# Kernel tuning notes

Measured on AMD Instinct MI355X. Metric: run time of the kernel, lower is better.

## Reference

```python
import jax, jax.numpy as jnp
import numpy as np

H = 64           # num_attention_heads
DH = 96          # attention_head_size = 6144/64
DM = 6144        # hidden_size


def setup_inputs() -> dict:
    key = jax.random.key(0)
    ks = jax.random.split(key, 7)
    s = 1.0 / np.sqrt(DM)
    return {
        "hidden_states": jax.random.normal(ks[0], (1, 2048, DM), dtype=jnp.float32),
        "Wq": jax.random.uniform(ks[1], (DM, DM), jnp.float32, -s, s),
        "bq": jax.random.uniform(ks[2], (DM,), jnp.float32, -s, s),
        "Wk": jax.random.uniform(ks[3], (DM, DM), jnp.float32, -s, s),
        "bk": jax.random.uniform(ks[4], (DM,), jnp.float32, -s, s),
        "Wv": jax.random.uniform(ks[5], (DM, DM), jnp.float32, -s, s),
        "bv": jax.random.uniform(ks[6], (DM,), jnp.float32, -s, s),
    }


def reference(hidden_states, Wq, bq, Wk, bk, Wv, bv):
    B, S, _ = hidden_states.shape

    def split_heads(x):  # [B,S,DM] -> [B,H,S,DH]
        return x.reshape(B, S, H, DH).transpose(0, 2, 1, 3)

    q = split_heads(hidden_states @ Wq + bq)
    k = split_heads(hidden_states @ Wk + bk)
    v = split_heads(hidden_states @ Wv + bv)

    scores = jnp.einsum("bhqd,bhkd->bhqk", q, k) / np.sqrt(DH).astype(np.float32)
    probs = jax.nn.softmax(scores, axis=-1)  # dropout p=0.0005 -> eval identity
    ctx = jnp.einsum("bhqk,bhkd->bhqd", probs, v)
    ctx = ctx.transpose(0, 2, 1, 3).reshape(B, S, H * DH)
    return ctx
```

## Files before the change

kernel.cpp:

```cpp
#include <hip/hip_runtime.h>
#include <hip/hip_bf16.h>
#include <stdint.h>


#define NH  64
#define DHD 96
#define DM  6144
#define SEQ 2048

typedef __attribute__((ext_vector_type(4))) float f4;
typedef __attribute__((ext_vector_type(4))) float f32x4;
typedef __attribute__((ext_vector_type(8))) short bf16x8;
typedef __attribute__((ext_vector_type(4))) short bf16x4;

static __device__ __forceinline__ short f2bf(float f) {
  unsigned int u = __builtin_bit_cast(unsigned int, f);
  u = (u + 0x7fffu + ((u >> 16) & 1u)) >> 16;
  return (short)u;
}

__global__ __launch_bounds__(256)
void qkv_gemm(const float* __restrict__ hs,
              const float* __restrict__ Wq, const float* __restrict__ bq,
              const float* __restrict__ Wk, const float* __restrict__ bk,
              const float* __restrict__ Wv, const float* __restrict__ bv,
              short* __restrict__ Qo, short* __restrict__ Ko, short* __restrict__ Vto)
{
  const int z = blockIdx.z;
  const float* __restrict__ Wp = (z == 0) ? Wq : ((z == 1) ? Wk : Wv);
  const float* __restrict__ bp = (z == 0) ? bq : ((z == 1) ? bk : bv);

  const int tid  = threadIdx.x;
  const int lane = tid & 63;
  const int w    = tid >> 6;
  const int wr   = w >> 1, wc = w & 1;
  const int g    = lane >> 4, c = lane & 15;
  const int m0   = blockIdx.y * 128;
  const int n0   = blockIdx.x * 128;

  __shared__ short Al[128 * 72];
  __shared__ short Bl[128 * 72];

  f32x4 acc[4][4];
#pragma unroll
  for (int i = 0; i < 4; ++i)
#pragma unroll
    for (int j = 0; j < 4; ++j) acc[i][j] = (f32x4)0.f;

  const int nb  = tid & 31;
  const int kb8 = tid >> 5;

  f4 areg[8];
  f4 breg[8];

  {
#pragma unroll
    for (int i = 0; i < 4; ++i) {
      int o = tid * 32 + i * 8192;
      int row = o >> 8, colf = (o & 255) >> 2;
      const float* p = hs + (size_t)(m0 + row) * DM + colf;
      areg[2*i]   = *(const f4*)p;
      areg[2*i+1] = *(const f4*)(p + 4);
    }
#pragma unroll
    for (int kk = 0; kk < 8; ++kk)
      breg[kk] = *(const f4*)(Wp + (size_t)(kb8*8 + kk) * DM + n0 + nb*4);
  }

  for (int kt = 0; kt < DM/64; ++kt) {
#pragma unroll
    for (int i = 0; i < 4; ++i) {
      int o = tid * 32 + i * 8192;
      int row = o >> 8, colf = (o & 255) >> 2;
      bf16x8 v;
      v[0]=f2bf(areg[2*i][0]);   v[1]=f2bf(areg[2*i][1]);
      v[2]=f2bf(areg[2*i][2]);   v[3]=f2bf(areg[2*i][3]);
      v[4]=f2bf(areg[2*i+1][0]); v[5]=f2bf(areg[2*i+1][1]);
      v[6]=f2bf(areg[2*i+1][2]); v[7]=f2bf(areg[2*i+1][3]);
      *(bf16x8*)&Al[row * 72 + colf] = v;
    }
#pragma unroll
    for (int nn = 0; nn < 4; ++nn) {
      bf16x8 v;
#pragma unroll
      for (int kk = 0; kk < 8; ++kk) v[kk] = f2bf(breg[kk][nn]);
      *(bf16x8*)&Bl[(nb*4 + nn) * 72 + kb8*8] = v;
    }
    __syncthreads();

    if (kt + 1 < DM/64) {
      const int k0 = (kt + 1) * 64;
#pragma unroll
      for (int i = 0; i < 4; ++i) {
        int o = tid * 32 + i * 8192;
        int row = o >> 8, colf = (o & 255) >> 2;
        const float* p = hs + (size_t)(m0 + row) * DM + k0 + colf;
        areg[2*i]   = *(const f4*)p;
        areg[2*i+1] = *(const f4*)(p + 4);
      }
#pragma unroll
      for (int kk = 0; kk < 8; ++kk)
        breg[kk] = *(const f4*)(Wp + (size_t)(k0 + kb8*8 + kk) * DM + n0 + nb*4);
    }

#pragma unroll
    for (int kh = 0; kh < 2; ++kh) {
      bf16x8 af[4], bfr[4];
#pragma unroll
      for (int i = 0; i < 4; ++i)
        af[i]  = *(bf16x8*)&Al[(wr*64 + i*16 + c) * 72 + kh*32 + g*8];
#pragma unroll
      for (int j = 0; j < 4; ++j)
        bfr[j] = *(bf16x8*)&Bl[(wc*64 + j*16 + c) * 72 + kh*32 + g*8];
#pragma unroll
      for (int i = 0; i < 4; ++i)
#pragma unroll
        for (int j = 0; j < 4; ++j)
          acc[i][j] = __builtin_amdgcn_mfma_f32_16x16x32_bf16(af[i], bfr[j], acc[i][j], 0, 0, 0);
    }
    __syncthreads();
  }

  if (z < 2) {
    short* __restrict__ outp = (z == 0) ? Qo : Ko;
#pragma unroll
    for (int j = 0; j < 4; ++j) {
      int n = n0 + wc*64 + j*16 + c;
      int hh = n / DHD, d = n - hh * DHD;
      float bias = bp[n];
      short* ob = outp + (size_t)hh * SEQ * DHD + d;
#pragma unroll
      for (int i = 0; i < 4; ++i) {
        int srow = m0 + wr*64 + i*16 + g*4;
#pragma unroll
        for (int r = 0; r < 4; ++r)
          ob[(size_t)(srow + r) * DHD] = f2bf(acc[i][j][r] + bias);
      }
    }
  } else {
#pragma unroll
    for (int j = 0; j < 4; ++j) {
      int n = n0 + wc*64 + j*16 + c;
      int hh = n / DHD, d = n - hh * DHD;
      float bias = bp[n];
      short* ob = Vto + ((size_t)hh * DHD + d) * SEQ;
#pragma unroll
      for (int i = 0; i < 4; ++i) {
        int srow = m0 + wr*64 + i*16 + g*4;
        bf16x4 v;
        v[0]=f2bf(acc[i][j][0]+bias); v[1]=f2bf(acc[i][j][1]+bias);
        v[2]=f2bf(acc[i][j][2]+bias); v[3]=f2bf(acc[i][j][3]+bias);
        *(bf16x4*)&ob[srow] = v;
      }
    }
  }
}

__global__ __launch_bounds__(256)
void attn_fwd(const short* __restrict__ Qo, const short* __restrict__ Ko,
              const short* __restrict__ Vto, float* __restrict__ out)
{
  const int h  = blockIdx.y;
  const int q0 = blockIdx.x * 64;
  const int tid = threadIdx.x, lane = tid & 63, w = tid >> 6;
  const int g = lane >> 4, c = lane & 15;

  __shared__ short Ql[64 * 104];
  __shared__ short Kl[64 * 104];
  __shared__ short Vl[96 * 72];
  __shared__ short Pl[64 * 72];

  const short* __restrict__ Qh = Qo  + (size_t)h * SEQ * DHD;
  const short* __restrict__ Kh = Ko  + (size_t)h * SEQ * DHD;
  const short* __restrict__ Vh = Vto + (size_t)h * DHD * SEQ;

#pragma unroll
  for (int j = 0; j < 3; ++j) {
    int i = tid + j * 256;
    int row = i / 12, cb = (i % 12) * 8;
    *(int4*)&Ql[row * 104 + cb] = *(const int4*)(Qh + (size_t)(q0 + row) * DHD + cb);
  }
  __syncthreads();

  bf16x8 qf[3];
#pragma unroll
  for (int dc = 0; dc < 3; ++dc)
    qf[dc] = *(bf16x8*)&Ql[(w*16 + c) * 104 + dc*32 + g*8];

  f32x4 octx[6];
#pragma unroll
  for (int i = 0; i < 6; ++i) octx[i] = (f32x4)0.f;
  float mrun = -__builtin_inff();
  float lrun = 0.f;
  const float rs = 0.10206207261596577f;

  for (int kv = 0; kv < SEQ/64; ++kv) {
    const int s0 = kv * 64;
    int4 kreg[3], vreg[3];
#pragma unroll
    for (int j = 0; j < 3; ++j) {
      int i = tid + j * 256;
      int krow = i / 12, kcb = (i % 12) * 8;
      kreg[j] = *(const int4*)(Kh + (size_t)(s0 + krow) * DHD + kcb);
      int vrow = i >> 3, vcb = (i & 7) * 8;
      vreg[j] = *(const int4*)(Vh + (size_t)vrow * SEQ + s0 + vcb);
    }
    __syncthreads();
#pragma unroll
    for (int j = 0; j < 3; ++j) {
      int i = tid + j * 256;
      int krow = i / 12, kcb = (i % 12) * 8;
      *(int4*)&Kl[krow * 104 + kcb] = kreg[j];
      int vrow = i >> 3, vcb = (i & 7) * 8;
      *(int4*)&Vl[vrow * 72 + vcb] = vreg[j];
    }
    __syncthreads();

    f32x4 sc[4];
#pragma unroll
    for (int kt = 0; kt < 4; ++kt) {
      sc[kt] = (f32x4)0.f;
#pragma unroll
      for (int dc = 0; dc < 3; ++dc) {
        bf16x8 kf = *(bf16x8*)&Kl[(kt*16 + c) * 104 + dc*32 + g*8];
        sc[kt] = __builtin_amdgcn_mfma_f32_16x16x32_bf16(kf, qf[dc], sc[kt], 0, 0, 0);
      }
    }

    float tmax = -__builtin_inff();
#pragma unroll
    for (int kt = 0; kt < 4; ++kt)
#pragma unroll
      for (int r = 0; r < 4; ++r) { sc[kt][r] *= rs; tmax = fmaxf(tmax, sc[kt][r]); }
    tmax = fmaxf(tmax, __shfl_xor(tmax, 16));
    tmax = fmaxf(tmax, __shfl_xor(tmax, 32));
    float mnew = fmaxf(mrun, tmax);
    float cs = __expf(mrun - mnew);
    float p[4][4];
    float psum = 0.f;
#pragma unroll
    for (int kt = 0; kt < 4; ++kt)
#pragma unroll
      for (int r = 0; r < 4; ++r) { p[kt][r] = __expf(sc[kt][r] - mnew); psum += p[kt][r]; }
    psum += __shfl_xor(psum, 16);
    psum += __shfl_xor(psum, 32);
    lrun = lrun * cs + psum;
    mrun = mnew;

    float csr[4];
#pragma unroll
    for (int r = 0; r < 4; ++r) csr[r] = __shfl(cs, g*4 + r, 64);
#pragma unroll
    for (int dt = 0; dt < 6; ++dt)
#pragma unroll
      for (int r = 0; r < 4; ++r) octx[dt][r] *= csr[r];

#pragma unroll
    for (int kt = 0; kt < 4; ++kt) {
      bf16x4 pv;
      pv[0]=f2bf(p[kt][0]); pv[1]=f2bf(p[kt][1]); pv[2]=f2bf(p[kt][2]); pv[3]=f2bf(p[kt][3]);
      *(bf16x4*)&Pl[(w*16 + c) * 72 + kt*16 + g*4] = pv;
    }
    asm volatile("s_waitcnt lgkmcnt(0)" ::: "memory");

    bf16x8 pa[2];
#pragma unroll
    for (int kh = 0; kh < 2; ++kh)
      pa[kh] = *(bf16x8*)&Pl[(w*16 + c) * 72 + kh*32 + g*8];
#pragma unroll
    for (int dt = 0; dt < 6; ++dt)
#pragma unroll
      for (int kh = 0; kh < 2; ++kh) {
        bf16x8 vf = *(bf16x8*)&Vl[(dt*16 + c) * 72 + kh*32 + g*8];
        octx[dt] = __builtin_amdgcn_mfma_f32_16x16x32_bf16(pa[kh], vf, octx[dt], 0, 0, 0);
      }
  }

  float rl = 1.f / lrun;
  float rlr[4];
#pragma unroll
  for (int r = 0; r < 4; ++r) rlr[r] = __shfl(rl, g*4 + r, 64);
#pragma unroll
  for (int dt = 0; dt < 6; ++dt) {
    int d = dt*16 + c;
#pragma unroll
    for (int r = 0; r < 4; ++r) {
      int srow = q0 + w*16 + g*4 + r;
      out[(size_t)srow * DM + h * DHD + d] = octx[dt][r] * rlr[r];
    }
  }
}

extern "C" void kernel_launch(void* const* d_in, const int* in_sizes, int n_in,
                              void* d_out, int out_size, void* d_ws, size_t ws_size,
                              hipStream_t stream) {
  const float* hs = (const float*)d_in[0];
  const float* Wq = (const float*)d_in[1];
  const float* bq = (const float*)d_in[2];
  const float* Wk = (const float*)d_in[3];
  const float* bk = (const float*)d_in[4];
  const float* Wv = (const float*)d_in[5];
  const float* bv = (const float*)d_in[6];

  short* Qo = (short*)d_ws;
  short* Ko = Qo + (size_t)NH * SEQ * DHD;
  short* Vt = Ko + (size_t)NH * SEQ * DHD;

  qkv_gemm<<<dim3(48, 16, 3), 256, 0, stream>>>(hs, Wq, bq, Wk, bk, Wv, bv, Qo, Ko, Vt);
  attn_fwd<<<dim3(SEQ/64, NH), 256, 0, stream>>>(Qo, Ko, Vt, (float*)d_out);
}
```

Measured before the change: 1.721 ms.

## Pre-convert inputs to bf16, use direct-to-LDS loads in GEMM, pipeline attention

The activations are converted to bf16 in a separate pass, and each weight matrix is converted and transposed into a bf16 workspace. The GEMM then streams tiles into LDS with global_load_lds and uses 512 threads per block. The attention kernel gains a block-index swizzle, register prefetch of the next K/V tile, priority hints around MFMA sections, and a lazy softmax rescale that is skipped when the max grows by 8 or less. These changes aim to remove in-loop fp32 conversion and strided weight reads, at the cost of extra conversion kernels and workspace traffic. The GEMM loop is single-buffered with no overlap of loads and compute.

```diff
diff --git a/kernel.cpp b/kernel.cpp
--- a/kernel.cpp
+++ b/kernel.cpp
@@ -13,6 +13,9 @@
 typedef __attribute__((ext_vector_type(8))) short bf16x8;
 typedef __attribute__((ext_vector_type(4))) short bf16x4;
 
+#define GLB(p) ((const __attribute__((address_space(1))) void*)(p))
+#define LDSP(p) ((__attribute__((address_space(3))) void*)(p))
+
 static __device__ __forceinline__ short f2bf(float f) {
   unsigned int u = __builtin_bit_cast(unsigned int, f);
   u = (u + 0x7fffu + ((u >> 16) & 1u)) >> 16;
@@ -20,100 +23,92 @@
 }
 
 __global__ __launch_bounds__(256)
-void qkv_gemm(const float* __restrict__ hs,
-              const float* __restrict__ Wq, const float* __restrict__ bq,
-              const float* __restrict__ Wk, const float* __restrict__ bk,
-              const float* __restrict__ Wv, const float* __restrict__ bv,
-              short* __restrict__ Qo, short* __restrict__ Ko, short* __restrict__ Vto)
+void conv_bf16(const float* __restrict__ in, short* __restrict__ out, int n8)
 {
-  const int z = blockIdx.z;
-  const float* __restrict__ Wp = (z == 0) ? Wq : ((z == 1) ? Wk : Wv);
-  const float* __restrict__ bp = (z == 0) ? bq : ((z == 1) ? bk : bv);
-
+  int stride = gridDim.x * 256;
+  for (int i = blockIdx.x * 256 + threadIdx.x; i < n8; i += stride) {
+    f4 a = *(const f4*)(in + (size_t)i * 8);
+    f4 b = *(const f4*)(in + (size_t)i * 8 + 4);
+    bf16x8 v;
+    v[0]=f2bf(a[0]); v[1]=f2bf(a[1]); v[2]=f2bf(a[2]); v[3]=f2bf(a[3]);
+    v[4]=f2bf(b[0]); v[5]=f2bf(b[1]); v[6]=f2bf(b[2]); v[7]=f2bf(b[3]);
+    *(bf16x8*)(out + (size_t)i * 8) = v;
+  }
+}
+
+__global__ __launch_bounds__(256)
+void conv_wt(const float* __restrict__ W, short* __restrict__ Wt, int n_base)
+{
+  __shared__ short T[64 * 72];
+  const int n0 = blockIdx.x * 64, k0 = blockIdx.y * 64;
+  const int t = threadIdx.x;
+  const int rr = t >> 4;
+  const int cc = (t & 15) * 4;
+#pragma unroll
+  for (int p = 0; p < 4; ++p) {
+    int r = rr + p * 16;
+    f4 a = *(const f4*)(W + (size_t)(k0 + r) * DM + n_base + n0 + cc);
+    T[(cc+0) * 72 + r] = f2bf(a[0]);
+    T[(cc+1) * 72 + r] = f2bf(a[1]);
+    T[(cc+2) * 72 + r] = f2bf(a[2]);
+    T[(cc+3) * 72 + r] = f2bf(a[3]);
+  }
+  __syncthreads();
+  const int n  = t >> 2;
+  const int kq = (t & 3) * 16;
+  *(int4*)(Wt + (size_t)(n0 + n) * DM + k0 + kq)     = *(const int4*)&T[n * 72 + kq];
+  *(int4*)(Wt + (size_t)(n0 + n) * DM + k0 + kq + 8) = *(const int4*)&T[n * 72 + kq + 8];
+}
+
+__global__ __launch_bounds__(512)
+void qkv_gemm(const short* __restrict__ Abf, const short* __restrict__ Bt,
+              const float* __restrict__ bp,
+              short* __restrict__ outQK, short* __restrict__ outVt, int isV, int n_base)
+{
   const int tid  = threadIdx.x;
   const int lane = tid & 63;
   const int w    = tid >> 6;
   const int wr   = w >> 1, wc = w & 1;
   const int g    = lane >> 4, c = lane & 15;
   const int m0   = blockIdx.y * 128;
-  const int n0   = blockIdx.x * 128;
-
-  __shared__ short Al[128 * 72];
-  __shared__ short Bl[128 * 72];
-
-  f32x4 acc[4][4];
-#pragma unroll
-  for (int i = 0; i < 4; ++i)
+  const int n0l  = blockIdx.x * 128;
+
+  __shared__ short Al[128 * 64];
+  __shared__ short Bl[128 * 64];
+
+  f32x4 acc[2][4];
+#pragma unroll
+  for (int i = 0; i < 2; ++i)
 #pragma unroll
     for (int j = 0; j < 4; ++j) acc[i][j] = (f32x4)0.f;
 
-  const int nb  = tid & 31;
-  const int kb8 = tid >> 5;
-
-  f4 areg[8];
-  f4 breg[8];
-
-  {
-#pragma unroll
-    for (int i = 0; i < 4; ++i) {
-      int o = tid * 32 + i * 8192;
-      int row = o >> 8, colf = (o & 255) >> 2;
-      const float* p = hs + (size_t)(m0 + row) * DM + colf;
-      areg[2*i]   = *(const f4*)p;
-      areg[2*i+1] = *(const f4*)(p + 4);
-    }
-#pragma unroll
-    for (int kk = 0; kk < 8; ++kk)
-      breg[kk] = *(const f4*)(Wp + (size_t)(kb8*8 + kk) * DM + n0 + nb*4);
-  }
-
-  for (int kt = 0; kt < DM/64; ++kt) {
-#pragma unroll
-    for (int i = 0; i < 4; ++i) {
-      int o = tid * 32 + i * 8192;
-      int row = o >> 8, colf = (o & 255) >> 2;
-      bf16x8 v;
-      v[0]=f2bf(areg[2*i][0]);   v[1]=f2bf(areg[2*i][1]);
-      v[2]=f2bf(areg[2*i][2]);   v[3]=f2bf(areg[2*i][3]);
-      v[4]=f2bf(areg[2*i+1][0]); v[5]=f2bf(areg[2*i+1][1]);
-      v[6]=f2bf(areg[2*i+1][2]); v[7]=f2bf(areg[2*i+1][3]);
-      *(bf16x8*)&Al[row * 72 + colf] = v;
-    }
-#pragma unroll
-    for (int nn = 0; nn < 4; ++nn) {
-      bf16x8 v;
-#pragma unroll
-      for (int kk = 0; kk < 8; ++kk) v[kk] = f2bf(breg[kk][nn]);
-      *(bf16x8*)&Bl[(nb*4 + nn) * 72 + kb8*8] = v;
+  const int cr   = lane >> 3;
+  const int ccol = (lane & 7) * 8;
+  const short* As = Abf + (size_t)(m0  + w*8 + cr) * DM + ccol;
+  const short* Bs = Bt  + (size_t)(n0l + w*8 + cr) * DM + ccol;
+  short* Adst = Al + w * 512;
+  short* Bdst = Bl + w * 512;
+
+  for (int kt = 0; kt < DM / 64; ++kt) {
+    const int ko = kt * 64;
+#pragma unroll
+    for (int i = 0; i < 2; ++i) {
+      __builtin_amdgcn_global_load_lds(GLB(As + (size_t)i * 64 * DM + ko), LDSP(Adst + i * 4096), 16, 0, 0);
+      __builtin_amdgcn_global_load_lds(GLB(Bs + (size_t)i * 64 * DM + ko), LDSP(Bdst + i * 4096), 16, 0, 0);
     }
     __syncthreads();
 
-    if (kt + 1 < DM/64) {
-      const int k0 = (kt + 1) * 64;
-#pragma unroll
-      for (int i = 0; i < 4; ++i) {
-        int o = tid * 32 + i * 8192;
-        int row = o >> 8, colf = (o & 255) >> 2;
-        const float* p = hs + (size_t)(m0 + row) * DM + k0 + colf;
-        areg[2*i]   = *(const f4*)p;
-        areg[2*i+1] = *(const f4*)(p + 4);
-      }
-#pragma unroll
-      for (int kk = 0; kk < 8; ++kk)
-        breg[kk] = *(const f4*)(Wp + (size_t)(k0 + kb8*8 + kk) * DM + n0 + nb*4);
-    }
-
 #pragma unroll
     for (int kh = 0; kh < 2; ++kh) {
-      bf16x8 af[4], bfr[4];
-#pragma unroll
-      for (int i = 0; i < 4; ++i)
-        af[i]  = *(bf16x8*)&Al[(wr*64 + i*16 + c) * 72 + kh*32 + g*8];
+      bf16x8 af[2], bfr[4];
+#pragma unroll
+      for (int i = 0; i < 2; ++i)
+        af[i]  = *(const bf16x8*)&Al[(wr*32 + i*16 + c) * 64 + kh*32 + g*8];
 #pragma unroll
       for (int j = 0; j < 4; ++j)
-        bfr[j] = *(bf16x8*)&Bl[(wc*64 + j*16 + c) * 72 + kh*32 + g*8];
-#pragma unroll
-      for (int i = 0; i < 4; ++i)
+        bfr[j] = *(const bf16x8*)&Bl[(wc*64 + j*16 + c) * 64 + kh*32 + g*8];
+#pragma unroll
+      for (int i = 0; i < 2; ++i)
 #pragma unroll
         for (int j = 0; j < 4; ++j)
           acc[i][j] = __builtin_amdgcn_mfma_f32_16x16x32_bf16(af[i], bfr[j], acc[i][j], 0, 0, 0);
@@ -121,36 +116,35 @@
     __syncthreads();
   }
 
-  if (z < 2) {
-    short* __restrict__ outp = (z == 0) ? Qo : Ko;
+  if (!isV) {
 #pragma unroll
     for (int j = 0; j < 4; ++j) {
-      int n = n0 + wc*64 + j*16 + c;
+      int n = n_base + n0l + wc*64 + j*16 + c;
       int hh = n / DHD, d = n - hh * DHD;
       float bias = bp[n];
-      short* ob = outp + (size_t)hh * SEQ * DHD + d;
-#pragma unroll
-      for (int i = 0; i < 4; ++i) {
-        int srow = m0 + wr*64 + i*16 + g*4;
+      short* ob = outQK + (size_t)hh * SEQ * DHD + d;
+#pragma unroll
+      for (int i = 0; i < 2; ++i) {
+        int srw = m0 + wr*32 + i*16 + g*4;
 #pragma unroll
         for (int r = 0; r < 4; ++r)
-          ob[(size_t)(srow + r) * DHD] = f2bf(acc[i][j][r] + bias);
+          ob[(size_t)(srw + r) * DHD] = f2bf(acc[i][j][r] + bias);
       }
     }
   } else {
 #pragma unroll
     for (int j = 0; j < 4; ++j) {
-      int n = n0 + wc*64 + j*16 + c;
+      int n = n_base + n0l + wc*64 + j*16 + c;
       int hh = n / DHD, d = n - hh * DHD;
       float bias = bp[n];
-      short* ob = Vto + ((size_t)hh * DHD + d) * SEQ;
-#pragma unroll
-      for (int i = 0; i < 4; ++i) {
-        int srow = m0 + wr*64 + i*16 + g*4;
+      short* ob = outVt + ((size_t)hh * DHD + d) * SEQ;
+#pragma unroll
+      for (int i = 0; i < 2; ++i) {
+        int srw = m0 + wr*32 + i*16 + g*4;
         bf16x4 v;
         v[0]=f2bf(acc[i][j][0]+bias); v[1]=f2bf(acc[i][j][1]+bias);
         v[2]=f2bf(acc[i][j][2]+bias); v[3]=f2bf(acc[i][j][3]+bias);
-        *(bf16x4*)&ob[srow] = v;
+        *(bf16x4*)&ob[srw] = v;
       }
     }
   }
@@ -160,8 +154,10 @@
 void attn_fwd(const short* __restrict__ Qo, const short* __restrict__ Ko,
               const short* __restrict__ Vto, float* __restrict__ out)
 {
-  const int h  = blockIdx.y;
-  const int q0 = blockIdx.x * 64;
+  const int b   = blockIdx.x;
+  const int swz = (b & 7) * (2048 / 8) + (b >> 3);
+  const int h   = swz >> 5;
+  const int q0  = (swz & 31) * 64;
   const int tid = threadIdx.x, lane = tid & 63, w = tid >> 6;
   const int g = lane >> 4, c = lane & 15;
 
@@ -185,7 +181,7 @@
   bf16x8 qf[3];
 #pragma unroll
   for (int dc = 0; dc < 3; ++dc)
-    qf[dc] = *(bf16x8*)&Ql[(w*16 + c) * 104 + dc*32 + g*8];
+    qf[dc] = *(const bf16x8*)&Ql[(w*16 + c) * 104 + dc*32 + g*8];
 
   f32x4 octx[6];
 #pragma unroll
@@ -194,17 +190,17 @@
   float lrun = 0.f;
   const float rs = 0.10206207261596577f;
 
-  for (int kv = 0; kv < SEQ/64; ++kv) {
-    const int s0 = kv * 64;
-    int4 kreg[3], vreg[3];
-#pragma unroll
-    for (int j = 0; j < 3; ++j) {
-      int i = tid + j * 256;
-      int krow = i / 12, kcb = (i % 12) * 8;
-      kreg[j] = *(const int4*)(Kh + (size_t)(s0 + krow) * DHD + kcb);
-      int vrow = i >> 3, vcb = (i & 7) * 8;
-      vreg[j] = *(const int4*)(Vh + (size_t)vrow * SEQ + s0 + vcb);
-    }
+  int4 kreg[3], vreg[3];
+#pragma unroll
+  for (int j = 0; j < 3; ++j) {
+    int i = tid + j * 256;
+    int krow = i / 12, kcb = (i % 12) * 8;
+    kreg[j] = *(const int4*)(Kh + (size_t)krow * DHD + kcb);
+    int vrow = i >> 3, vcb = (i & 7) * 8;
+    vreg[j] = *(const int4*)(Vh + (size_t)vrow * SEQ + vcb);
+  }
+
+  for (int kv = 0; kv < SEQ / 64; ++kv) {
     __syncthreads();
 #pragma unroll
     for (int j = 0; j < 3; ++j) {
@@ -216,16 +212,30 @@
     }
     __syncthreads();
 
+    if (kv + 1 < SEQ / 64) {
+      const int s1 = (kv + 1) * 64;
+#pragma unroll
+      for (int j = 0; j < 3; ++j) {
+        int i = tid + j * 256;
+        int krow = i / 12, kcb = (i % 12) * 8;
+        kreg[j] = *(const int4*)(Kh + (size_t)(s1 + krow) * DHD + kcb);
+        int vrow = i >> 3, vcb = (i & 7) * 8;
+        vreg[j] = *(const int4*)(Vh + (size_t)vrow * SEQ + s1 + vcb);
+      }
+    }
+
     f32x4 sc[4];
+    __builtin_amdgcn_s_setprio(1);
 #pragma unroll
     for (int kt = 0; kt < 4; ++kt) {
       sc[kt] = (f32x4)0.f;
 #pragma unroll
       for (int dc = 0; dc < 3; ++dc) {
-        bf16x8 kf = *(bf16x8*)&Kl[(kt*16 + c) * 104 + dc*32 + g*8];
+        bf16x8 kf = *(const bf16x8*)&Kl[(kt*16 + c) * 104 + dc*32 + g*8];
         sc[kt] = __builtin_amdgcn_mfma_f32_16x16x32_bf16(kf, qf[dc], sc[kt], 0, 0, 0);
       }
     }
+    __builtin_amdgcn_s_setprio(0);
 
     float tmax = -__builtin_inff();
 #pragma unroll
@@ -234,26 +244,28 @@
       for (int r = 0; r < 4; ++r) { sc[kt][r] *= rs; tmax = fmaxf(tmax, sc[kt][r]); }
     tmax = fmaxf(tmax, __shfl_xor(tmax, 16));
     tmax = fmaxf(tmax, __shfl_xor(tmax, 32));
-    float mnew = fmaxf(mrun, tmax);
-    float cs = __expf(mrun - mnew);
+    if (!__all(tmax - mrun <= 8.0f)) {
+      float mnew = fmaxf(mrun, tmax);
+      float cs = __expf(mrun - mnew);
+      mrun = mnew;
+      lrun *= cs;
+      float csr[4];
+#pragma unroll
+      for (int r = 0; r < 4; ++r) csr[r] = __shfl(cs, g*4 + r, 64);
+#pragma unroll
+      for (int dt = 0; dt < 6; ++dt)
+#pragma unroll
+        for (int r = 0; r < 4; ++r) octx[dt][r] *= csr[r];
+    }
     float p[4][4];
     float psum = 0.f;
 #pragma unroll
     for (int kt = 0; kt < 4; ++kt)
 #pragma unroll
-      for (int r = 0; r < 4; ++r) { p[kt][r] = __expf(sc[kt][r] - mnew); psum += p[kt][r]; }
+      for (int r = 0; r < 4; ++r) { p[kt][r] = __expf(sc[kt][r] - mrun); psum += p[kt][r]; }
     psum += __shfl_xor(psum, 16);
     psum += __shfl_xor(psum, 32);
-    lrun = lrun * cs + psum;
-    mrun = mnew;
-
-    float csr[4];
-#pragma unroll
-    for (int r = 0; r < 4; ++r) csr[r] = __shfl(cs, g*4 + r, 64);
-#pragma unroll
-    for (int dt = 0; dt < 6; ++dt)
-#pragma unroll
-      for (int r = 0; r < 4; ++r) octx[dt][r] *= csr[r];
+    lrun += psum;
 
 #pragma unroll
     for (int kt = 0; kt < 4; ++kt) {
@@ -262,18 +274,21 @@
       *(bf16x4*)&Pl[(w*16 + c) * 72 + kt*16 + g*4] = pv;
     }
     asm volatile("s_waitcnt lgkmcnt(0)" ::: "memory");
+    __builtin_amdgcn_sched_barrier(0);
 
     bf16x8 pa[2];
 #pragma unroll
     for (int kh = 0; kh < 2; ++kh)
-      pa[kh] = *(bf16x8*)&Pl[(w*16 + c) * 72 + kh*32 + g*8];
+      pa[kh] = *(const bf16x8*)&Pl[(w*16 + c) * 72 + kh*32 + g*8];
+    __builtin_amdgcn_s_setprio(1);
 #pragma unroll
     for (int dt = 0; dt < 6; ++dt)
 #pragma unroll
       for (int kh = 0; kh < 2; ++kh) {
-        bf16x8 vf = *(bf16x8*)&Vl[(dt*16 + c) * 72 + kh*32 + g*8];
+        bf16x8 vf = *(const bf16x8*)&Vl[(dt*16 + c) * 72 + kh*32 + g*8];
         octx[dt] = __builtin_amdgcn_mfma_f32_16x16x32_bf16(pa[kh], vf, octx[dt], 0, 0, 0);
       }
+    __builtin_amdgcn_s_setprio(0);
   }
 
   float rl = 1.f / lrun;
@@ -295,17 +310,36 @@
                               void* d_out, int out_size, void* d_ws, size_t ws_size,
                               hipStream_t stream) {
   const float* hs = (const float*)d_in[0];
-  const float* Wq = (const float*)d_in[1];
-  const float* bq = (const float*)d_in[2];
-  const float* Wk = (const float*)d_in[3];
-  const float* bk = (const float*)d_in[4];
-  const float* Wv = (const float*)d_in[5];
-  const float* bv = (const float*)d_in[6];
+  const float* Ws[3] = { (const float*)d_in[1], (const float*)d_in[3], (const float*)d_in[5] };
+  const float* bs[3] = { (const float*)d_in[2], (const float*)d_in[4], (const float*)d_in[6] };
 
   short* Qo = (short*)d_ws;
   short* Ko = Qo + (size_t)NH * SEQ * DHD;
   short* Vt = Ko + (size_t)NH * SEQ * DHD;
-
-  qkv_gemm<<<dim3(48, 16, 3), 256, 0, stream>>>(hs, Wq, bq, Wk, bk, Wv, bv, Qo, Ko, Vt);
-  attn_fwd<<<dim3(SEQ/64, NH), 256, 0, stream>>>(Qo, Ko, Vt, (float*)d_out);
-}
+  short* outs[3] = { Qo, Ko, Vt };
+
+  const size_t FULL_BYTES = 3ull*NH*SEQ*DHD*2 + (size_t)SEQ*DM*2 + (size_t)DM*DM*2;
+
+  if (ws_size >= FULL_BYTES) {
+    short* Abf = Vt  + (size_t)NH * SEQ * DHD;
+    short* Wtb = Abf + (size_t)SEQ * DM;
+    conv_bf16<<<2048, 256, 0, stream>>>(hs, Abf, SEQ * DM / 8);
+    for (int z = 0; z < 3; ++z) {
+      conv_wt<<<dim3(96, 96), 256, 0, stream>>>(Ws[z], Wtb, 0);
+      qkv_gemm<<<dim3(48, 16), 512, 0, stream>>>(Abf, Wtb, bs[z],
+          (z < 2) ? outs[z] : nullptr, (z == 2) ? Vt : nullptr, z == 2, 0);
+    }
+  } else {
+    short* Abf = (short*)d_out;
+    short* Wts = Abf + (size_t)SEQ * DM;
+    conv_bf16<<<2048, 256, 0, stream>>>(hs, Abf, SEQ * DM / 8);
+    for (int z = 0; z < 3; ++z)
+      for (int s = 0; s < 3; ++s) {
+        conv_wt<<<dim3(32, 96), 256, 0, stream>>>(Ws[z], Wts, s * 2048);
+        qkv_gemm<<<dim3(16, 16), 512, 0, stream>>>(Abf, Wts, bs[z],
+            (z < 2) ? outs[z] : nullptr, (z == 2) ? Vt : nullptr, z == 2, s * 2048);
+      }
+  }
+
+  attn_fwd<<<2048, 256, 0, stream>>>(Qo, Ko, Vt, (float*)d_out);
+}
```

Result: faster. 1.643 ms (-4.5%).
